# Optimization experiments

Hardware: AMD Instinct MI355X
Metric: run time of the kernel (lower is better)

## Reference

```python
import jax, jax.numpy as jnp
import numpy as np

D_MODEL, D_FF, N_EXPERTS, TOP_K = 1024, 4096, 8, 2
B, S = 4, 1024
EPS = 1e-5

def setup_inputs() -> dict:
    key = jax.random.key(0)
    ks = jax.random.split(key, 8)
    sd = 1.0 / np.sqrt(D_MODEL)
    sf = 1.0 / np.sqrt(D_FF)
    return {
        "x": jax.random.normal(ks[0], (B, S, D_MODEL), dtype=jnp.float32),
        "mask": jnp.ones((B, S), dtype=bool),
        "Wg": jax.random.normal(ks[1], (D_MODEL, N_EXPERTS), dtype=jnp.float32) * sd,
        "W1": jax.random.normal(ks[2], (N_EXPERTS, D_MODEL, D_FF), dtype=jnp.float32) * sd,
        "b1": jnp.zeros((N_EXPERTS, D_FF), dtype=jnp.float32),
        "W2": jax.random.normal(ks[3], (N_EXPERTS, D_FF, D_MODEL), dtype=jnp.float32) * sf,
        "b2": jnp.zeros((N_EXPERTS, D_MODEL), dtype=jnp.float32),
        "gamma": jnp.ones((D_MODEL,), dtype=jnp.float32),
        "beta": jnp.zeros((D_MODEL,), dtype=jnp.float32),
    }

def _layernorm(x, gamma, beta):
    mu = jnp.mean(x, axis=-1, keepdims=True)
    var = jnp.mean(jnp.square(x - mu), axis=-1, keepdims=True)
    return (x - mu) * jax.lax.rsqrt(var + EPS) * gamma + beta

def reference(x, mask, Wg, W1, b1, W2, b2, gamma, beta):
    Bq, Sq, D = x.shape
    T = Bq * Sq
    xf = x.reshape(T, D)                       # [T, D]
    logits = xf @ Wg                           # [T, E]
    probs = jax.nn.softmax(logits, axis=-1)
    topv, topi = jax.lax.top_k(probs, TOP_K)   # [T, K]
    w = topv / jnp.sum(topv, axis=-1, keepdims=True)
    combine = jnp.zeros((T, N_EXPERTS), dtype=probs.dtype)
    combine = combine.at[jnp.arange(T)[:, None], topi].add(w)  # [T, E]
    # all-expert FFN (dense reference for grouped expert GEMMs)
    h = jax.nn.relu(jnp.einsum('td,edf->tef', xf, W1) + b1)    # [T, E, F]
    ye = jnp.einsum('tef,efd->ted', h, W2) + b2                # [T, E, D]
    y = jnp.einsum('te,ted->td', combine, ye)                  # [T, D]
    # load-balancing aux loss (Switch-style)
    frac_tokens = jnp.mean((combine > 0).astype(probs.dtype), axis=0)  # [E]
    frac_probs = jnp.mean(probs, axis=0)                                # [E]
    aux_loss = N_EXPERTS * jnp.sum(frac_tokens * frac_probs)
    out = _layernorm(x + y.reshape(Bq, Sq, D), gamma, beta)
    return out, aux_loss
```

## Files before the change

### kernel.cpp

```cpp
#include <hip/hip_runtime.h>
#include <cstdint>
#include <cstddef>


#define T_TOK 4096
#define DM 1024
#define DF 4096
#define NE 8
#define CAP 9216
#define MAXMT 72

typedef __bf16 bf16;
typedef __bf16 bf16x2 __attribute__((ext_vector_type(2)));
typedef __bf16 bf16x4 __attribute__((ext_vector_type(4)));
typedef __bf16 bf16x8 __attribute__((ext_vector_type(8)));
typedef float f32x4 __attribute__((ext_vector_type(4)));

struct Meta {
  int pad_off[NE + 1];
  int n_mtiles;
  int tile_e[80];
  int tile_m0[80];
};

__global__ __launch_bounds__(256) void router_kernel(
    const float* __restrict__ x, const float* __restrict__ Wg,
    int* __restrict__ topi, float* __restrict__ topw, float* __restrict__ probs) {
  int wave = threadIdx.x >> 6, lane = threadIdx.x & 63;
  int t = blockIdx.x * 4 + wave;
  const float* xr = x + (size_t)t * DM;
  float acc[NE];
#pragma unroll
  for (int e = 0; e < NE; e++) acc[e] = 0.f;
  for (int d0 = 0; d0 < DM; d0 += 64) {
    float xv = xr[d0 + lane];
    const float4* wrow = (const float4*)(Wg + (size_t)(d0 + lane) * NE);
    float4 w0 = wrow[0], w1 = wrow[1];
    acc[0] += xv * w0.x; acc[1] += xv * w0.y; acc[2] += xv * w0.z; acc[3] += xv * w0.w;
    acc[4] += xv * w1.x; acc[5] += xv * w1.y; acc[6] += xv * w1.z; acc[7] += xv * w1.w;
  }
#pragma unroll
  for (int off = 32; off >= 1; off >>= 1) {
#pragma unroll
    for (int e = 0; e < NE; e++) acc[e] += __shfl_xor(acc[e], off);
  }
  if (lane == 0) {
    float m = acc[0];
#pragma unroll
    for (int e = 1; e < NE; e++) m = fmaxf(m, acc[e]);
    float p[NE], s = 0.f;
#pragma unroll
    for (int e = 0; e < NE; e++) { p[e] = expf(acc[e] - m); s += p[e]; }
    float inv = 1.f / s;
#pragma unroll
    for (int e = 0; e < NE; e++) { p[e] *= inv; probs[t * NE + e] = p[e]; }
    int i1 = 0; float v1 = acc[0];
#pragma unroll
    for (int e = 1; e < NE; e++) if (acc[e] > v1) { v1 = acc[e]; i1 = e; }
    int i2 = -1; float v2 = -1e30f;
#pragma unroll
    for (int e = 0; e < NE; e++) if (e != i1 && acc[e] > v2) { v2 = acc[e]; i2 = e; }
    float sw = p[i1] + p[i2];
    topi[t * 2] = i1; topi[t * 2 + 1] = i2;
    topw[t * 2] = p[i1] / sw; topw[t * 2 + 1] = p[i2] / sw;
  }
}

__global__ __launch_bounds__(256) void prep_kernel(
    const int* __restrict__ topi, const float* __restrict__ probs,
    Meta* __restrict__ meta, float* __restrict__ aux_out) {
  __shared__ int scnt[NE];
  __shared__ float wps[4][NE];
  int tid = threadIdx.x, lane = tid & 63, wave = tid >> 6;
  if (tid < NE) scnt[tid] = 0;
  __syncthreads();
  for (int i = tid; i < T_TOK * 2; i += 256) atomicAdd(&scnt[topi[i]], 1);
  float lp[NE];
#pragma unroll
  for (int e = 0; e < NE; e++) lp[e] = 0.f;
  for (int tt = tid; tt < T_TOK; tt += 256) {
#pragma unroll
    for (int e = 0; e < NE; e++) lp[e] += probs[tt * NE + e];
  }
#pragma unroll
  for (int off = 32; off >= 1; off >>= 1) {
#pragma unroll
    for (int e = 0; e < NE; e++) lp[e] += __shfl_xor(lp[e], off);
  }
  if (lane == 0) {
#pragma unroll
    for (int e = 0; e < NE; e++) wps[wave][e] = lp[e];
  }
  __syncthreads();
  if (tid == 0) {
    float aux = 0.f;
    int nt = 0, po = 0;
    for (int e = 0; e < NE; e++) {
      float ps = wps[0][e] + wps[1][e] + wps[2][e] + wps[3][e];
      aux += (float)scnt[e] * ps;
      meta->pad_off[e] = po;
      int pc = (scnt[e] + 127) & ~127;
      for (int i = 0; i < pc / 128; i++) {
        meta->tile_e[nt] = e; meta->tile_m0[nt] = po + i * 128; nt++;
      }
      po += pc;
    }
    meta->pad_off[NE] = po;
    meta->n_mtiles = nt;
    aux_out[0] = aux * (8.f / ((float)T_TOK * (float)T_TOK));
  }
}

__global__ __launch_bounds__(64) void scatter_kernel(
    const int* __restrict__ topi, const float* __restrict__ topw,
    const Meta* __restrict__ meta,
    int* __restrict__ t_of, float* __restrict__ w_of, int* __restrict__ k_of) {
  int e = blockIdx.x, lane = threadIdx.x;
  int base = meta->pad_off[e];
  for (int c = 0; c < T_TOK * 2; c += 64) {
    int idx = c + lane;
    int sel = (topi[idx] == e) ? 1 : 0;
    unsigned long long mask = __ballot(sel);
    if (sel) {
      int rank = __popcll(mask & ((1ull << lane) - 1ull));
      int s = base + rank;
      t_of[s] = idx >> 1;
      k_of[s] = idx & 1;
      w_of[s] = topw[idx];
    }
    base += (int)__popcll(mask);
  }
}

__global__ __launch_bounds__(256) void gather_kernel(
    const float* __restrict__ x, const int* __restrict__ t_of,
    unsigned short* __restrict__ Xg_u) {
  int s = blockIdx.x;
  int t = t_of[s];
  if (t < 0) return;
  bf16* Xg = (bf16*)Xg_u;
  int i = threadIdx.x;
  float4 v = ((const float4*)(x + (size_t)t * DM))[i];
  bf16x4 o = {(bf16)v.x, (bf16)v.y, (bf16)v.z, (bf16)v.w};
  ((bf16x4*)(Xg + (size_t)s * DM))[i] = o;
}

__global__ __launch_bounds__(256) void transpose_kernel(
    const float* __restrict__ src, unsigned short* __restrict__ dst_u, int R, int C) {
  bf16* dst = (bf16*)dst_u;
  int e = blockIdx.z;
  int c0 = blockIdx.x * 32, r0 = blockIdx.y * 32;
  int tx = threadIdx.x & 31, ty = threadIdx.x >> 5;
  __shared__ float tile[32][33];
  const float* s = src + (size_t)e * R * C;
#pragma unroll
  for (int j = 0; j < 32; j += 8)
    tile[ty + j][tx] = s[(size_t)(r0 + ty + j) * C + c0 + tx];
  __syncthreads();
  bf16* d = dst + (size_t)e * C * R;
  int wr_ = threadIdx.x & 15;
  int wc_ = threadIdx.x >> 4;
#pragma unroll
  for (int j = 0; j < 32; j += 16) {
    int c = wc_ + j;
    bf16x2 v = {(bf16)tile[2 * wr_][c], (bf16)tile[2 * wr_ + 1][c]};
    *(bf16x2*)&d[(size_t)(c0 + c) * R + r0 + 2 * wr_] = v;
  }
}

__device__ inline void gl_lds16(const void* g, void* l) {
  __builtin_amdgcn_global_load_lds(
      (const __attribute__((address_space(1))) unsigned int*)g,
      (__attribute__((address_space(3))) unsigned int*)l, 16, 0, 0);
}

template <int MODE>
__global__ __launch_bounds__(256) void gemm_kernel(
    const unsigned short* __restrict__ A_u, const unsigned short* __restrict__ Bt_u,
    const float* __restrict__ bias, const Meta* __restrict__ meta,
    int Ktot, int Ksp, int N,
    unsigned short* __restrict__ Hout_u,
    float* __restrict__ P0, float* __restrict__ P1,
    const int* __restrict__ t_of, const int* __restrict__ k_of,
    const float* __restrict__ w_of) {
  int bx = blockIdx.x;
  if (bx >= meta->n_mtiles) return;
  const bf16* A = (const bf16*)A_u;
  const bf16* Bt = (const bf16*)Bt_u;
  int e = meta->tile_e[bx];
  int m0 = meta->tile_m0[bx];
  int n0 = blockIdx.y * 128;
  int koff = blockIdx.z * Ksp;
  const bf16* Be = Bt + (size_t)e * N * Ktot;

  __shared__ bf16 As[128 * 64];
  __shared__ bf16 Bs[128 * 64];

  int tid = threadIdx.x, lane = tid & 63, wave = tid >> 6;
  int wr = wave >> 1, wc = wave & 1;
  int srow = lane >> 3;
  int sgran = lane & 7;
  int gcol = (sgran ^ srow) * 8;

  const bf16* Ag = A + (size_t)(m0 + wave * 8 + srow) * Ktot + koff + gcol;
  const bf16* Bg = Be + (size_t)(n0 + wave * 8 + srow) * Ktot + koff + gcol;
  bf16* AsW = As + wave * 512;
  bf16* BsW = Bs + wave * 512;

  f32x4 acc[4][4];
#pragma unroll
  for (int i = 0; i < 4; i++)
#pragma unroll
    for (int j = 0; j < 4; j++) acc[i][j] = (f32x4){0.f, 0.f, 0.f, 0.f};

  int fr = lane & 15;
  int qh = lane >> 4;
  int swz = fr & 7;

  for (int k0 = 0; k0 < Ksp; k0 += 64) {
#pragma unroll
    for (int r = 0; r < 4; r++) {
      gl_lds16(Ag + (size_t)(r * 32) * Ktot + k0, AsW + r * 2048);
      gl_lds16(Bg + (size_t)(r * 32) * Ktot + k0, BsW + r * 2048);
    }
    __syncthreads();
#pragma unroll
    for (int kk = 0; kk < 64; kk += 32) {
      int col = (((kk >> 3) | qh) ^ swz) * 8;
      bf16x8 af[4], bfr[4];
#pragma unroll
      for (int i = 0; i < 4; i++)
        af[i] = *(const bf16x8*)&As[(wr * 64 + i * 16 + fr) * 64 + col];
#pragma unroll
      for (int j = 0; j < 4; j++)
        bfr[j] = *(const bf16x8*)&Bs[(wc * 64 + j * 16 + fr) * 64 + col];
#pragma unroll
      for (int i = 0; i < 4; i++)
#pragma unroll
        for (int j = 0; j < 4; j++)
          acc[i][j] = __builtin_amdgcn_mfma_f32_16x16x32_bf16(af[i], bfr[j], acc[i][j], 0, 0, 0);
    }
    __syncthreads();
  }

  int crow = (lane >> 4) * 4;
  int ccol = lane & 15;
  if (MODE == 1) {
    bf16* Hout = (bf16*)Hout_u;
#pragma unroll
    for (int i = 0; i < 4; i++) {
#pragma unroll
      for (int r = 0; r < 4; r++) {
        int slot = m0 + wr * 64 + i * 16 + crow + r;
        bf16* hrow = Hout + (size_t)slot * N;
#pragma unroll
        for (int j = 0; j < 4; j++) {
          int n = n0 + wc * 64 + j * 16 + ccol;
          float v = acc[i][j][r] + bias[e * N + n];
          hrow[n] = (bf16)fmaxf(v, 0.f);
        }
      }
    }
  } else {
    float* Pz = (blockIdx.z == 0) ? P0 : P1;
    int addb = (blockIdx.z == 0) ? 1 : 0;
#pragma unroll
    for (int i = 0; i < 4; i++) {
#pragma unroll
      for (int r = 0; r < 4; r++) {
        int slot = m0 + wr * 64 + i * 16 + crow + r;
        int t = t_of[slot];
        if (t < 0) continue;
        int ks = k_of[slot];
        float w = w_of[slot];
        float* yrow = Pz + ((size_t)ks * T_TOK + t) * DM;
#pragma unroll
        for (int j = 0; j < 4; j++) {
          int n = n0 + wc * 64 + j * 16 + ccol;
          float bv = addb ? bias[e * DM + n] : 0.f;
          yrow[n] = (acc[i][j][r] + bv) * w;
        }
      }
    }
  }
}

__global__ __launch_bounds__(256) void ln_kernel(
    const float* __restrict__ x,
    const float* __restrict__ P0, const float* __restrict__ P1,
    const float* __restrict__ gamma, const float* __restrict__ beta,
    float* __restrict__ out) {
  int t = blockIdx.x, tid = threadIdx.x, lane = tid & 63, wave = tid >> 6;
  size_t row = (size_t)t * DM;
  size_t kstride = (size_t)T_TOK * DM;
  float4 a  = ((const float4*)(x + row))[tid];
  float4 y0 = ((const float4*)(P0 + row))[tid];
  float4 y1 = ((const float4*)(P0 + kstride + row))[tid];
  float4 y2 = ((const float4*)(P1 + row))[tid];
  float4 y3 = ((const float4*)(P1 + kstride + row))[tid];
  float4 sv;
  sv.x = a.x + y0.x + y1.x + y2.x + y3.x;
  sv.y = a.y + y0.y + y1.y + y2.y + y3.y;
  sv.z = a.z + y0.z + y1.z + y2.z + y3.z;
  sv.w = a.w + y0.w + y1.w + y2.w + y3.w;
  float sum = sv.x + sv.y + sv.z + sv.w;
  float sq = sv.x * sv.x + sv.y * sv.y + sv.z * sv.z + sv.w * sv.w;
#pragma unroll
  for (int off = 32; off >= 1; off >>= 1) {
    sum += __shfl_xor(sum, off);
    sq += __shfl_xor(sq, off);
  }
  __shared__ float ls[4], lq[4], stats[2];
  if (lane == 0) { ls[wave] = sum; lq[wave] = sq; }
  __syncthreads();
  if (tid == 0) {
    float ts = ls[0] + ls[1] + ls[2] + ls[3];
    float tq = lq[0] + lq[1] + lq[2] + lq[3];
    float mu = ts * (1.f / DM);
    float var = tq * (1.f / DM) - mu * mu;
    stats[0] = mu;
    stats[1] = rsqrtf(var + 1e-5f);
  }
  __syncthreads();
  float mu = stats[0], rs = stats[1];
  float4 g = ((const float4*)gamma)[tid];
  float4 b = ((const float4*)beta)[tid];
  float4 o;
  o.x = (sv.x - mu) * rs * g.x + b.x;
  o.y = (sv.y - mu) * rs * g.y + b.y;
  o.z = (sv.z - mu) * rs * g.z + b.z;
  o.w = (sv.w - mu) * rs * g.w + b.w;
  ((float4*)(out + row))[tid] = o;
}

extern "C" void kernel_launch(void* const* d_in, const int* in_sizes, int n_in,
                              void* d_out, int out_size, void* d_ws, size_t ws_size,
                              hipStream_t stream) {
  const float* x     = (const float*)d_in[0];
  const float* Wg    = (const float*)d_in[2];
  const float* W1    = (const float*)d_in[3];
  const float* b1    = (const float*)d_in[4];
  const float* W2    = (const float*)d_in[5];
  const float* b2    = (const float*)d_in[6];
  const float* gamma = (const float*)d_in[7];
  const float* beta  = (const float*)d_in[8];
  float* out = (float*)d_out;

  char* ws = (char*)d_ws;
  size_t off = 0;
  auto alloc = [&](size_t bytes) -> void* {
    off = (off + 4095) & ~(size_t)4095;
    void* p = ws + off;
    off += bytes;
    return p;
  };
  Meta* meta   = (Meta*)alloc(sizeof(Meta));
  int* topi    = (int*)alloc((size_t)T_TOK * 2 * 4);
  float* topw  = (float*)alloc((size_t)T_TOK * 2 * 4);
  float* probs = (float*)alloc((size_t)T_TOK * NE * 4);
  int* t_of    = (int*)alloc((size_t)CAP * 4);
  int* k_of    = (int*)alloc((size_t)CAP * 4);
  float* w_of  = (float*)alloc((size_t)CAP * 4);
  size_t xg_bytes = (size_t)CAP * DM * 2;
  size_t p_bytes  = (size_t)2 * T_TOK * DM * 4;
  char* xg_region = (char*)alloc(xg_bytes > p_bytes ? xg_bytes : p_bytes);
  unsigned short* Xg = (unsigned short*)xg_region;
  float* Psp1        = (float*)xg_region;
  unsigned short* Hbuf = (unsigned short*)alloc((size_t)CAP * DF * 2);
  float* Psp0          = (float*)alloc(p_bytes);
  unsigned short* WT   = (unsigned short*)alloc((size_t)NE * DM * DF * 2);

  hipMemsetAsync(t_of, 0xFF, (size_t)CAP * 4, stream);

  router_kernel<<<dim3(T_TOK / 4), dim3(256), 0, stream>>>(x, Wg, topi, topw, probs);
  prep_kernel<<<dim3(1), dim3(256), 0, stream>>>(topi, probs, meta, out + (size_t)T_TOK * DM);
  scatter_kernel<<<dim3(NE), dim3(64), 0, stream>>>(topi, topw, meta, t_of, w_of, k_of);
  gather_kernel<<<dim3(CAP), dim3(256), 0, stream>>>(x, t_of, Xg);

  transpose_kernel<<<dim3(DF / 32, DM / 32, NE), dim3(256), 0, stream>>>(W1, WT, DM, DF);
  gemm_kernel<1><<<dim3(MAXMT, DF / 128, 1), dim3(256), 0, stream>>>(
      Xg, WT, b1, meta, DM, DM, DF, Hbuf, (float*)nullptr, (float*)nullptr,
      (const int*)nullptr, (const int*)nullptr, (const float*)nullptr);

  transpose_kernel<<<dim3(DM / 32, DF / 32, NE), dim3(256), 0, stream>>>(W2, WT, DF, DM);
  gemm_kernel<2><<<dim3(MAXMT, DM / 128, 2), dim3(256), 0, stream>>>(
      Hbuf, WT, b2, meta, DF, DF / 2, DM, (unsigned short*)nullptr, Psp0, Psp1,
      t_of, k_of, w_of);

  ln_kernel<<<dim3(T_TOK), dim3(256), 0, stream>>>(x, Psp0, Psp1, gamma, beta, out);
}
```

Baseline: 674.6 us.

## Remap GEMM blocks per XCD for L2 reuse and widen weight transpose tiles

The GEMM kernels now decode a linear block id so that the tiles sharing an XCD (id mod 8) cover a contiguous range of M-tiles, aiming to improve L2 reuse of A and B operands across the chiplet layout. The weight transpose kernel moves to 64x64 tiles with float4 global loads and 16-byte bf16x8 stores, replacing scalar loads and 4-byte stores. Both changes target memory-traffic efficiency. The remap assumes gridDim.x is divisible by 8 (MAXMT=72), and the padded shared tile may still see some bank conflicts on column reads.

```diff
diff --git a/kernel.cpp b/kernel.cpp
--- a/kernel.cpp
+++ b/kernel.cpp
@@ -11,7 +11,6 @@
 #define MAXMT 72
 
 typedef __bf16 bf16;
-typedef __bf16 bf16x2 __attribute__((ext_vector_type(2)));
 typedef __bf16 bf16x4 __attribute__((ext_vector_type(4)));
 typedef __bf16 bf16x8 __attribute__((ext_vector_type(8)));
 typedef float f32x4 __attribute__((ext_vector_type(4)));
@@ -149,22 +148,30 @@
     const float* __restrict__ src, unsigned short* __restrict__ dst_u, int R, int C) {
   bf16* dst = (bf16*)dst_u;
   int e = blockIdx.z;
-  int c0 = blockIdx.x * 32, r0 = blockIdx.y * 32;
-  int tx = threadIdx.x & 31, ty = threadIdx.x >> 5;
-  __shared__ float tile[32][33];
+  int c0 = blockIdx.x * 64, r0 = blockIdx.y * 64;
+  __shared__ float tile[64][69];
   const float* s = src + (size_t)e * R * C;
-#pragma unroll
-  for (int j = 0; j < 32; j += 8)
-    tile[ty + j][tx] = s[(size_t)(r0 + ty + j) * C + c0 + tx];
+  int lr = threadIdx.x >> 4;
+  int lc4 = (threadIdx.x & 15) * 4;
+#pragma unroll
+  for (int p = 0; p < 4; p++) {
+    float4 v = *(const float4*)&s[(size_t)(r0 + p * 16 + lr) * C + c0 + lc4];
+    tile[p * 16 + lr][lc4]     = v.x;
+    tile[p * 16 + lr][lc4 + 1] = v.y;
+    tile[p * 16 + lr][lc4 + 2] = v.z;
+    tile[p * 16 + lr][lc4 + 3] = v.w;
+  }
   __syncthreads();
   bf16* d = dst + (size_t)e * C * R;
-  int wr_ = threadIdx.x & 15;
-  int wc_ = threadIdx.x >> 4;
-#pragma unroll
-  for (int j = 0; j < 32; j += 16) {
-    int c = wc_ + j;
-    bf16x2 v = {(bf16)tile[2 * wr_][c], (bf16)tile[2 * wr_ + 1][c]};
-    *(bf16x2*)&d[(size_t)(c0 + c) * R + r0 + 2 * wr_] = v;
+#pragma unroll
+  for (int s2 = 0; s2 < 2; s2++) {
+    int q = threadIdx.x + 256 * s2;
+    int c = q >> 3;
+    int rs = (q & 7) * 8;
+    bf16x8 o;
+#pragma unroll
+    for (int j = 0; j < 8; j++) o[j] = (bf16)tile[rs + j][c];
+    *(bf16x8*)&d[(size_t)(c0 + c) * R + r0 + rs] = o;
   }
 }
 
@@ -183,14 +190,21 @@
     float* __restrict__ P0, float* __restrict__ P1,
     const int* __restrict__ t_of, const int* __restrict__ k_of,
     const float* __restrict__ w_of) {
-  int bx = blockIdx.x;
+  int id = blockIdx.x + gridDim.x * (blockIdx.y + gridDim.y * blockIdx.z);
+  int xcd = id & 7;
+  int rr = id >> 3;
+  int chunk = gridDim.x >> 3;
+  int bx = xcd * chunk + rr % chunk;
+  int rest = rr / chunk;
+  int n0 = (rest % gridDim.y) * 128;
+  int bz = rest / gridDim.y;
+
   if (bx >= meta->n_mtiles) return;
   const bf16* A = (const bf16*)A_u;
   const bf16* Bt = (const bf16*)Bt_u;
   int e = meta->tile_e[bx];
   int m0 = meta->tile_m0[bx];
-  int n0 = blockIdx.y * 128;
-  int koff = blockIdx.z * Ksp;
+  int koff = bz * Ksp;
   const bf16* Be = Bt + (size_t)e * N * Ktot;
 
   __shared__ bf16 As[128 * 64];
@@ -262,8 +276,8 @@
       }
     }
   } else {
-    float* Pz = (blockIdx.z == 0) ? P0 : P1;
-    int addb = (blockIdx.z == 0) ? 1 : 0;
+    float* Pz = (bz == 0) ? P0 : P1;
+    int addb = (bz == 0) ? 1 : 0;
 #pragma unroll
     for (int i = 0; i < 4; i++) {
 #pragma unroll
@@ -377,12 +391,12 @@
   scatter_kernel<<<dim3(NE), dim3(64), 0, stream>>>(topi, topw, meta, t_of, w_of, k_of);
   gather_kernel<<<dim3(CAP), dim3(256), 0, stream>>>(x, t_of, Xg);
 
-  transpose_kernel<<<dim3(DF / 32, DM / 32, NE), dim3(256), 0, stream>>>(W1, WT, DM, DF);
+  transpose_kernel<<<dim3(DF / 64, DM / 64, NE), dim3(256), 0, stream>>>(W1, WT, DM, DF);
   gemm_kernel<1><<<dim3(MAXMT, DF / 128, 1), dim3(256), 0, stream>>>(
       Xg, WT, b1, meta, DM, DM, DF, Hbuf, (float*)nullptr, (float*)nullptr,
       (const int*)nullptr, (const int*)nullptr, (const float*)nullptr);
 
-  transpose_kernel<<<dim3(DM / 32, DF / 32, NE), dim3(256), 0, stream>>>(W2, WT, DF, DM);
+  transpose_kernel<<<dim3(DM / 64, DF / 64, NE), dim3(256), 0, stream>>>(W2, WT, DF, DM);
   gemm_kernel<2><<<dim3(MAXMT, DM / 128, 2), dim3(256), 0, stream>>>(
       Hbuf, WT, b2, meta, DF, DF / 2, DM, (unsigned short*)nullptr, Psp0, Psp1,
       t_of, k_of, w_of);
```

Result: faster. 643.4 us (-4.6%).
